# Optimization experiments

Hardware: AMD Instinct MI355X
Metric: run time of the kernel (lower is better)

## Reference

```python
import jax, jax.numpy as jnp
import numpy as np

N = 50000      # nodes
E = 800000     # edges
F_IN = 128     # numInputFeatures
HID = 64       # numHiddenLayerFeatures
C = 40         # numClasses


def setup_inputs() -> dict:
    key = jax.random.key(0)
    ks = jax.random.split(key, 24)
    def nrm(k, shape, s=0.05):
        return jax.random.normal(k, shape, jnp.float32) * s
    return {
        "x": jax.random.normal(ks[0], (N, F_IN), jnp.float32),
        "edge_index": jax.random.randint(ks[1], (2, E), 0, N, jnp.int64),
        "w": jax.random.normal(ks[2], (3,), jnp.float32),  # ensemble weights
        # GCNConv
        "W_gcn": nrm(ks[3], (F_IN, HID)), "b_gcn": jnp.zeros((HID,), jnp.float32),
        # SAGEConv (lin_l on aggregated neighbors w/ bias, lin_r on root no bias)
        "Wl_sage": nrm(ks[4], (F_IN, HID)), "bl_sage": jnp.zeros((HID,), jnp.float32),
        "Wr_sage": nrm(ks[5], (F_IN, HID)),
        # GATConv heads=1
        "W_gat": nrm(ks[6], (F_IN, HID)), "att_src": nrm(ks[7], (HID,)),
        "att_dst": nrm(ks[8], (HID,)), "b_gat": jnp.zeros((HID,), jnp.float32),
        # TransformerConv heads=1 (hidden -> classes)
        "Wq": nrm(ks[9], (HID, C)), "bq": jnp.zeros((C,), jnp.float32),
        "Wk": nrm(ks[10], (HID, C)), "bk": jnp.zeros((C,), jnp.float32),
        "Wv": nrm(ks[11], (HID, C)), "bv": jnp.zeros((C,), jnp.float32),
        "Wskip": nrm(ks[12], (HID, C)), "bskip": jnp.zeros((C,), jnp.float32),
    }


def _segment_softmax(e, seg, num_segments):
    m = jax.ops.segment_max(e, seg, num_segments=num_segments)
    ex = jnp.exp(e - m[seg])
    s = jax.ops.segment_sum(ex, seg, num_segments=num_segments)
    return ex / (s[seg] + 1e-16)


def _gcn(x, src, dst, W, b):
    h = x @ W                                        # [N, HID]
    loop = jnp.arange(N, dtype=src.dtype)
    s = jnp.concatenate([src, loop]); d = jnp.concatenate([dst, loop])
    deg = jax.ops.segment_sum(jnp.ones_like(d, jnp.float32), d, num_segments=N)
    dinv = jnp.where(deg > 0, jax.lax.rsqrt(deg), 0.0)
    norm = dinv[s] * dinv[d]                         # [E+N]
    out = jax.ops.segment_sum(h[s] * norm[:, None], d, num_segments=N)
    return out + b


def _sage(x, src, dst, Wl, bl, Wr):
    cnt = jax.ops.segment_sum(jnp.ones((src.shape[0],), jnp.float32), dst, num_segments=N)
    agg = jax.ops.segment_sum(x[src], dst, num_segments=N) / jnp.maximum(cnt, 1.0)[:, None]
    return agg @ Wl + bl + x @ Wr


def _gat(x, src, dst, W, att_src, att_dst, b):
    h = x @ W                                        # [N, HID]
    loop = jnp.arange(N, dtype=src.dtype)
    s = jnp.concatenate([src, loop]); d = jnp.concatenate([dst, loop])
    a_s = h @ att_src; a_d = h @ att_dst             # [N]
    e = jax.nn.leaky_relu(a_s[s] + a_d[d], 0.2)
    alpha = _segment_softmax(e, d, N)
    out = jax.ops.segment_sum(alpha[:, None] * h[s], d, num_segments=N)
    return out + b


def _transformer(x, src, dst, Wq, bq, Wk, bk, Wv, bv, Wskip, bskip):
    q = x @ Wq + bq; k = x @ Wk + bk; v = x @ Wv + bv  # [N, C]
    score = jnp.sum(q[dst] * k[src], axis=-1) / jnp.sqrt(jnp.float32(C))
    alpha = _segment_softmax(score, dst, N)
    out = jax.ops.segment_sum(alpha[:, None] * v[src], dst, num_segments=N)
    return out + (x @ Wskip + bskip)


def reference(x, edge_index, w, W_gcn, b_gcn, Wl_sage, bl_sage, Wr_sage,
              W_gat, att_src, att_dst, b_gat,
              Wq, bq, Wk, bk, Wv, bv, Wskip, bskip):
    src, dst = edge_index[0], edge_index[1]
    gelu = lambda t: jax.nn.gelu(t, approximate=False)
    ens = gelu(_gcn(x, src, dst, W_gcn, b_gcn)) * w[0]
    ens = ens + gelu(_sage(x, src, dst, Wl_sage, bl_sage, Wr_sage)) * w[1]
    ens = ens + gelu(_gat(x, src, dst, W_gat, att_src, att_dst, b_gat)) * w[2]
    out = _transformer(ens, src, dst, Wq, bq, Wk, bk, Wv, bv, Wskip, bskip)
    return jax.nn.log_softmax(out, axis=1)
```

## Files before the change

kernel.cpp:

```cpp
#include <hip/hip_runtime.h>
#include <math.h>

#define NN 50000
#define EE 800000
#define FIN 128
#define HID 64
#define CL 40
#define SCB 256
#define NBLK ((NN + SCB - 1) / SCB)
#define NREP 8
#define QW 256

typedef unsigned short ushort_t;
typedef unsigned int uint_t;
typedef float f32x2 __attribute__((ext_vector_type(2)));
typedef float f32x4 __attribute__((ext_vector_type(4)));
typedef short s16x8 __attribute__((ext_vector_type(8)));

#if defined(__has_builtin)
#if __has_builtin(__builtin_amdgcn_cvt_pk_f32_fp8)
#define HAVE_CVT_FP8 1
#endif
#endif

__device__ __forceinline__ ushort_t f2bf(float f) {
  uint_t u = __float_as_uint(f);
  u = (u + 0x7FFFu + ((u >> 16) & 1u)) >> 16;
  return (ushort_t)u;
}
__device__ __forceinline__ uint_t f2bf2(float lo, float hi) {
  return (uint_t)f2bf(lo) | ((uint_t)f2bf(hi) << 16);
}
__device__ __forceinline__ float bflo(uint_t u) {
  return __uint_as_float(u << 16);
}
__device__ __forceinline__ float bfhi(uint_t u) {
  return __uint_as_float(u & 0xFFFF0000u);
}

__device__ __forceinline__ uint_t f32_to_fp8(float f) {
  uint_t u = __float_as_uint(f);
  uint_t s = (u >> 31) << 7;
  uint_t mag = u & 0x7FFFFFFFu;
  if (mag < 0x3C800000u) return s;
  if (mag > 0x43E00000u) mag = 0x43E00000u;
  uint_t r = mag + 0x7FFFFu + ((mag >> 20) & 1u);
  if (r > 0x43E00000u) r = 0x43E00000u;
  return s | (((r - (120u << 23)) >> 20) & 0x7Fu);
}
__device__ __forceinline__ void fp8x4_to_f32(uint_t u, float* o) {
#ifdef HAVE_CVT_FP8
  f32x2 lo = __builtin_amdgcn_cvt_pk_f32_fp8(u, false);
  f32x2 hi = __builtin_amdgcn_cvt_pk_f32_fp8(u, true);
  o[0] = lo[0]; o[1] = lo[1]; o[2] = hi[0]; o[3] = hi[1];
#else
#pragma unroll
  for (int i = 0; i < 4; ++i) {
    uint_t b = (u >> (8 * i)) & 0xFFu;
    uint_t em = b & 0x7Fu;
    uint_t bits = ((b & 0x80u) << 24) | ((em << 20) + (120u << 23));
    o[i] = em ? __uint_as_float(bits) : 0.f;
  }
#endif
}

__device__ __forceinline__ int wave_sum_i(int v) {
#pragma unroll
  for (int off = 32; off > 0; off >>= 1) v += __shfl_xor(v, off, 64);
  return v;
}
__device__ __forceinline__ float wave_sum_f(float v) {
#pragma unroll
  for (int off = 32; off > 0; off >>= 1) v += __shfl_xor(v, off, 64);
  return v;
}
__device__ __forceinline__ float half_sum(float v) {
#pragma unroll
  for (int off = 16; off > 0; off >>= 1) v += __shfl_xor(v, off, 64);
  return v;
}
__device__ __forceinline__ float half_max(float v) {
#pragma unroll
  for (int off = 16; off > 0; off >>= 1) v = fmaxf(v, __shfl_xor(v, off, 64));
  return v;
}
__device__ __forceinline__ float gelu_exact(float x) {
  return 0.5f * x * (1.0f + erff(x * 0.70710678118654752f));
}
__device__ __forceinline__ float leaky02(float x) {
  return x >= 0.f ? x : 0.2f * x;
}

#define PREP_W 169
#define PREP_HIST 3125
#define PREP_X 12500
__global__ __launch_bounds__(256) void k_prep(
    const float* __restrict__ x, const int* __restrict__ dst,
    const float* __restrict__ W0, const float* __restrict__ W1,
    const float* __restrict__ W2, const float* __restrict__ W3,
    const float* __restrict__ Q0, const float* __restrict__ Q1,
    const float* __restrict__ Q2, const float* __restrict__ Q3,
    const float* __restrict__ b0, const float* __restrict__ b1,
    const float* __restrict__ b2, const float* __restrict__ b3,
    const float* __restrict__ attS, const float* __restrict__ attD,
    ushort_t* __restrict__ WtA, ushort_t* __restrict__ WtB,
    float* __restrict__ bcat, float* __restrict__ wv,
    int* __restrict__ cntR, int* __restrict__ erank,
    uint_t* __restrict__ xbu, ushort_t* __restrict__ xb8,
    float* __restrict__ a_s, float* __restrict__ a_d) {
  int b = blockIdx.x, t = threadIdx.x;
  if (b < PREP_W) {
    int idx = b * 256 + t;
    if (idx < 32768) {
      int m = idx >> 13, r = idx & 8191, c = r >> 7, k = r & 127;
      const float* W = (m == 0) ? W0 : (m == 1) ? W1 : (m == 2) ? W2 : W3;
      WtA[idx] = f2bf(W[k * HID + c]);
    } else if (idx < 43008) {
      int j = idx - 32768;
      int c = j >> 6, k = j & 63;
      int mm = c / CL, cc = c % CL;
      const float* W = (mm == 0) ? Q0 : (mm == 1) ? Q1 : (mm == 2) ? Q2 : Q3;
      WtB[j] = f2bf(W[k * CL + cc]);
    } else if (idx < 43168) {
      int c = idx - 43008;
      int mm = c / CL, cc = c % CL;
      const float* bb = (mm == 0) ? b0 : (mm == 1) ? b1 : (mm == 2) ? b2 : b3;
      bcat[c] = bb[cc];
    }
  } else if (b < PREP_W + PREP_HIST) {
    int hb = b - PREP_W;
    int e = hb * 256 + t;
    if (e < EE) {
      int r = hb & (NREP - 1);
      erank[e] = atomicAdd(&cntR[(size_t)r * NN + dst[e]], 1);
    }
  } else if (b < PREP_W + PREP_HIST + 1) {
    int which = t >> 7, k = t & 127;
    const float* att = which ? attD : attS;
    float s = 0.f;
    for (int c = 0; c < HID; ++c) s = fmaf(W2[k * HID + c], att[c], s);
    wv[which * FIN + k] = s;
  } else {
    int node = (b - PREP_W - PREP_HIST - 1) * 4 + (t >> 6);
    int l = t & 63;
    if (node < NN) {
      float2 xv = ((const float2*)x)[(size_t)node * 64 + l];
      float2 wsv = ((const float2*)wv)[l];
      float2 wdv = ((const float2*)(wv + FIN))[l];
      float ps = fmaf(xv.x, wsv.x, xv.y * wsv.y);
      float pd = fmaf(xv.x, wdv.x, xv.y * wdv.y);
      ps = wave_sum_f(ps);
      pd = wave_sum_f(pd);
      xbu[(size_t)node * 64 + l] = f2bf2(xv.x, xv.y);
      xb8[(size_t)node * 64 + l] =
          (ushort_t)(f32_to_fp8(xv.x) | (f32_to_fp8(xv.y) << 8));
      if (l == 0) { a_s[node] = ps; a_d[node] = pd; }
    }
  }
}

__global__ __launch_bounds__(SCB) void k_bsum(const int* __restrict__ cntR,
                                              int* __restrict__ bsum) {
  __shared__ int wsm[4];
  int i = blockIdx.x * SCB + threadIdx.x;
  int v = 0;
  if (i < NN) {
#pragma unroll
    for (int r = 0; r < NREP; ++r) v += cntR[(size_t)r * NN + i];
  }
  int s = wave_sum_i(v);
  int lane = threadIdx.x & 63, wv = threadIdx.x >> 6;
  if (lane == 0) wsm[wv] = s;
  __syncthreads();
  if (threadIdx.x == 0) bsum[blockIdx.x] = wsm[0] + wsm[1] + wsm[2] + wsm[3];
}

__global__ __launch_bounds__(SCB) void k_scanapply(
    const int* __restrict__ cntR, const int* __restrict__ bsum,
    const float* __restrict__ a_s, const float* __restrict__ a_d,
    int* __restrict__ cnt, int* __restrict__ offs, int* __restrict__ base8,
    float* __restrict__ dinv, float2* __restrict__ auxS,
    float2* __restrict__ auxD) {
  __shared__ int ts[SCB];
  __shared__ int wred[4];
  int b = blockIdx.x, t = threadIdx.x;
  int pv = (t < b) ? bsum[t] : 0;
  int ps = wave_sum_i(pv);
  int lane = t & 63, wv = t >> 6;
  if (lane == 0) wred[wv] = ps;
  int i = b * SCB + t;
  int cr[NREP];
  int v = 0;
  if (i < NN) {
#pragma unroll
    for (int r = 0; r < NREP; ++r) {
      cr[r] = cntR[(size_t)r * NN + i];
      v += cr[r];
    }
  }
  ts[t] = v;
  __syncthreads();
  int prefix = wred[0] + wred[1] + wred[2] + wred[3];
  for (int off = 1; off < SCB; off <<= 1) {
    int u = (t >= off) ? ts[t - off] : 0;
    __syncthreads();
    ts[t] += u;
    __syncthreads();
  }
  if (i < NN) {
    int ex = ts[t] - v + prefix;
    offs[i] = ex;
    cnt[i] = v;
    float dv = rsqrtf((float)v + 1.0f);
    dinv[i] = dv;
    auxS[i] = make_float2(dv, a_s[i]);
    auxD[i] = make_float2(dv, a_d[i]);
    int run = ex;
#pragma unroll
    for (int r = 0; r < NREP; ++r) {
      base8[(size_t)i * NREP + r] = run;
      run += cr[r];
    }
  }
}

__global__ __launch_bounds__(256) void k_sc1(const int* __restrict__ dst,
                                             const int* __restrict__ erank,
                                             const int* __restrict__ base8,
                                             int* __restrict__ esorted) {
  int e = blockIdx.x * blockDim.x + threadIdx.x;
  if (e < EE) {
    int d = dst[e];
    int r = (e >> 8) & (NREP - 1);
    esorted[base8[(size_t)d * NREP + r] + erank[e]] = e;
  }
}

__global__ __launch_bounds__(256) void k_sc2(
    const int* __restrict__ esorted, const int* __restrict__ src,
    const int* __restrict__ dst, const float2* __restrict__ auxS,
    const float2* __restrict__ auxD, int* __restrict__ srcidx,
    int* __restrict__ dsts, float2* __restrict__ edata) {
  int p = blockIdx.x * blockDim.x + threadIdx.x;
  if (p < EE) {
    int e = esorted[p];
    int s = src[e], d = dst[e];
    srcidx[p] = s;
    dsts[p] = d;
    float2 A = auxS[s];
    float2 B = auxD[d];
    float ex = __expf(leaky02(A.y + B.y));
    edata[p] = make_float2(A.x * B.x, ex);
  }
}

__global__ __launch_bounds__(256) void k_agg1x(
    const int* __restrict__ srcidx, const int* __restrict__ offs,
    const int* __restrict__ cnt, const uint_t* __restrict__ xb8u,
    const uint_t* __restrict__ xbu, const float2* __restrict__ edata,
    const float* __restrict__ dinv, const float* __restrict__ a_s,
    const float* __restrict__ a_d, uint_t* __restrict__ aggu) {
  int node = (blockIdx.x * blockDim.x + threadIdx.x) >> 6;
  int lane = threadIdx.x & 63;
  if (node >= NN) return;
  const int half = lane >> 5;
  const int fl = lane & 31;
  int beg = offs[node];
  int c = cnt[node];
  int end = beg + c;
  float g[4] = {0.f, 0.f, 0.f, 0.f};
  float sS[4] = {0.f, 0.f, 0.f, 0.f};
  float tA[4] = {0.f, 0.f, 0.f, 0.f};
  float dg = 0.f;
  int p = beg + half;
  for (; p + 6 < end; p += 8) {
    int s0 = srcidx[p], s1 = srcidx[p + 2], s2 = srcidx[p + 4],
        s3 = srcidx[p + 6];
    float2 e0 = edata[p], e1 = edata[p + 2], e2 = edata[p + 4],
           e3 = edata[p + 6];
    uint_t u0 = xb8u[(size_t)s0 * 32 + fl];
    uint_t u1 = xb8u[(size_t)s1 * 32 + fl];
    uint_t u2 = xb8u[(size_t)s2 * 32 + fl];
    uint_t u3 = xb8u[(size_t)s3 * 32 + fl];
    float A[4], B[4], C[4], D[4];
    fp8x4_to_f32(u0, A);
    fp8x4_to_f32(u1, B);
    fp8x4_to_f32(u2, C);
    fp8x4_to_f32(u3, D);
#pragma unroll
    for (int i = 0; i < 4; ++i) {
      g[i] = fmaf(A[i], e0.x, g[i]);
      g[i] = fmaf(B[i], e1.x, g[i]);
      g[i] = fmaf(C[i], e2.x, g[i]);
      g[i] = fmaf(D[i], e3.x, g[i]);
      sS[i] += (A[i] + B[i]) + (C[i] + D[i]);
      tA[i] = fmaf(A[i], e0.y, tA[i]);
      tA[i] = fmaf(B[i], e1.y, tA[i]);
      tA[i] = fmaf(C[i], e2.y, tA[i]);
      tA[i] = fmaf(D[i], e3.y, tA[i]);
    }
    dg += (e0.y + e1.y) + (e2.y + e3.y);
  }
  for (; p < end; p += 2) {
    int s0 = srcidx[p];
    float2 e0 = edata[p];
    uint_t u0 = xb8u[(size_t)s0 * 32 + fl];
    float A[4];
    fp8x4_to_f32(u0, A);
#pragma unroll
    for (int i = 0; i < 4; ++i) {
      g[i] = fmaf(A[i], e0.x, g[i]);
      sS[i] += A[i];
      tA[i] = fmaf(A[i], e0.y, tA[i]);
    }
    dg += e0.y;
  }
#pragma unroll
  for (int i = 0; i < 4; ++i) {
    g[i] += __shfl_xor(g[i], 32, 64);
    sS[i] += __shfl_xor(sS[i], 32, 64);
    tA[i] += __shfl_xor(tA[i], 32, 64);
  }
  dg += __shfl_xor(dg, 32, 64);
  float dd = dinv[node];
  float exl = __expf(leaky02(a_s[node] + a_d[node]));
  uint_t n0 = xbu[(size_t)node * 64 + 2 * fl];
  uint_t n1 = xbu[(size_t)node * 64 + 2 * fl + 1];
  float X[4] = {bflo(n0), bfhi(n0), bflo(n1), bfhi(n1)};
  float dd2 = dd * dd;
  float cinv = 1.0f / fmaxf((float)c, 1.0f);
  float gdi = 1.0f / (dg + exl + 1e-16f);
#pragma unroll
  for (int i = 0; i < 4; ++i) {
    g[i] = fmaf(X[i], dd2, g[i]);
    tA[i] = fmaf(X[i], exl, tA[i]);
    sS[i] *= cinv;
    tA[i] *= gdi;
  }
  if (half == 0) {
    uint_t* ag = aggu + (size_t)node * 192;
    ag[2 * fl] = f2bf2(g[0], g[1]);
    ag[2 * fl + 1] = f2bf2(g[2], g[3]);
    ag[64 + 2 * fl] = f2bf2(sS[0], sS[1]);
    ag[64 + 2 * fl + 1] = f2bf2(sS[2], sS[3]);
    ag[128 + 2 * fl] = f2bf2(tA[0], tA[1]);
    ag[128 + 2 * fl + 1] = f2bf2(tA[2], tA[3]);
  }
}

__global__ __launch_bounds__(256) void k_post(
    const ushort_t* __restrict__ agg, const ushort_t* __restrict__ xb,
    const ushort_t* __restrict__ WtA, const float* __restrict__ b_gcn,
    const float* __restrict__ bl, const float* __restrict__ b_gat,
    const float* __restrict__ w, ushort_t* __restrict__ ensb) {
  __shared__ __align__(16) ushort_t wlds[64 * 136];
  const int t = threadIdx.x;
  const int wv = t >> 6, l = t & 63;
  const int lr = l & 15, lg = l >> 4;
  const int rbase = blockIdx.x * 64 + wv * 16;
  int arow = rbase + lr;
  int arowc = arow < NN ? arow : NN - 1;
  f32x4 acc[4][4] = {};
#pragma unroll
  for (int m = 0; m < 4; ++m) {
    if (m) __syncthreads();
    for (int idx = t; idx < 64 * 16; idx += 256) {
      int c = idx >> 4, ch = idx & 15;
      *(uint4*)&wlds[c * 136 + ch * 8] =
          *(const uint4*)(WtA + m * 8192 + c * 128 + ch * 8);
    }
    __syncthreads();
    const ushort_t* ap = (m < 3) ? agg + (size_t)arowc * 384 + m * 128 + lg * 8
                                 : xb + (size_t)arowc * 128 + lg * 8;
#pragma unroll
    for (int ks = 0; ks < 4; ++ks) {
      s16x8 af = *(const s16x8*)(ap + ks * 32);
#pragma unroll
      for (int n = 0; n < 4; ++n) {
        s16x8 bf = *(const s16x8*)&wlds[(n * 16 + lr) * 136 + ks * 32 + lg * 8];
        acc[m][n] =
            __builtin_amdgcn_mfma_f32_16x16x32_bf16(af, bf, acc[m][n], 0, 0, 0);
      }
    }
  }
  float w0 = w[0], w1 = w[1], w2 = w[2];
#pragma unroll
  for (int n = 0; n < 4; ++n) {
    int col = n * 16 + lr;
    float bgv = b_gcn[col], bsv = bl[col], bav = b_gat[col];
#pragma unroll
    for (int j = 0; j < 4; ++j) {
      int orow = rbase + lg * 4 + j;
      if (orow < NN) {
        float g = gelu_exact(acc[0][n][j] + bgv);
        float s = gelu_exact(acc[1][n][j] + acc[3][n][j] + bsv);
        float tt = gelu_exact(acc[2][n][j] + bav);
        ensb[(size_t)orow * 64 + col] = f2bf(w0 * g + w1 * s + w2 * tt);
      }
    }
  }
}

__global__ __launch_bounds__(256) void k_gemmB(
    const ushort_t* __restrict__ ensb, const ushort_t* __restrict__ WtB,
    const float* __restrict__ bcat, ushort_t* __restrict__ QKVSb) {
  __shared__ __align__(16) ushort_t wb[160 * 72];
  __shared__ float bsh[160];
  const int t = threadIdx.x;
  for (int idx = t; idx < 160 * 8; idx += 256) {
    int c = idx >> 3, ch = idx & 7;
    *(uint4*)&wb[c * 72 + ch * 8] = *(const uint4*)(WtB + c * 64 + ch * 8);
  }
  if (t < 160) bsh[t] = bcat[t];
  __syncthreads();
  const int wv = t >> 6, l = t & 63;
  const int lr = l & 15, lg = l >> 4;
  const int rbase = blockIdx.x * 64 + wv * 16;
  int arow = rbase + lr;
  int arowc = arow < NN ? arow : NN - 1;
  const ushort_t* ap = ensb + (size_t)arowc * 64 + lg * 8;
  f32x4 acc[10] = {};
#pragma unroll
  for (int ks = 0; ks < 2; ++ks) {
    s16x8 af = *(const s16x8*)(ap + ks * 32);
#pragma unroll
    for (int n = 0; n < 10; ++n) {
      s16x8 bf = *(const s16x8*)&wb[(n * 16 + lr) * 72 + ks * 32 + lg * 8];
      acc[n] = __builtin_amdgcn_mfma_f32_16x16x32_bf16(af, bf, acc[n], 0, 0, 0);
    }
  }
#pragma unroll
  for (int n = 0; n < 10; ++n) {
    int col = n * 16 + lr;
    int seg = col / CL;
    int off = seg * 64 + (col - seg * CL);
#pragma unroll
    for (int j = 0; j < 4; ++j) {
      int orow = rbase + lg * 4 + j;
      if (orow < NN)
        QKVSb[(size_t)orow * QW + off] = f2bf(acc[n][j] + bsh[col]);
    }
  }
}

__global__ __launch_bounds__(256) void k_score(
    const int* __restrict__ srcidx, const int* __restrict__ dsts,
    const ushort_t* __restrict__ QKVSb, float* __restrict__ escore) {
  int p = blockIdx.x * 256 + threadIdx.x;
  if (p >= EE) return;
  int s = srcidx[p], d = dsts[p];
  const uint4* qp = (const uint4*)(QKVSb + (size_t)d * QW);
  const uint4* kp = (const uint4*)(QKVSb + (size_t)s * QW + 64);
  float dot = 0.f;
#pragma unroll
  for (int i = 0; i < 5; ++i) {
    uint4 q = qp[i], k = kp[i];
    dot = fmaf(bflo(q.x), bflo(k.x), dot);
    dot = fmaf(bfhi(q.x), bfhi(k.x), dot);
    dot = fmaf(bflo(q.y), bflo(k.y), dot);
    dot = fmaf(bfhi(q.y), bfhi(k.y), dot);
    dot = fmaf(bflo(q.z), bflo(k.z), dot);
    dot = fmaf(bfhi(q.z), bfhi(k.z), dot);
    dot = fmaf(bflo(q.w), bflo(k.w), dot);
    dot = fmaf(bfhi(q.w), bfhi(k.w), dot);
  }
  escore[p] = __expf(dot * 0.15811388300841897f);
}

__global__ __launch_bounds__(256) void k_agg2(
    const int* __restrict__ srcidx, const int* __restrict__ offs,
    const int* __restrict__ cnt, const ushort_t* __restrict__ QKVSb,
    const float* __restrict__ escore, float* __restrict__ out) {
  int node = (blockIdx.x * blockDim.x + threadIdx.x) >> 6;
  int lane = threadIdx.x & 63;
  if (node >= NN) return;
  const int half = lane >> 5;
  const int fl = lane & 31;
  const bool valid = fl < 20;
  int beg = offs[node];
  int end = beg + cnt[node];
  float den = 0.f, av0 = 0.f, av1 = 0.f;
  const int VOFF = 64;
  int p = beg + half;
  for (; p + 6 < end; p += 8) {
    int sA = srcidx[p], sB = srcidx[p + 2], sC = srcidx[p + 4],
        sD = srcidx[p + 6];
    float eA = escore[p], eB = escore[p + 2], eC = escore[p + 4],
          eD = escore[p + 6];
    uint_t vA = valid ? ((const uint_t*)QKVSb)[(size_t)sA * 128 + VOFF + fl] : 0u;
    uint_t vB = valid ? ((const uint_t*)QKVSb)[(size_t)sB * 128 + VOFF + fl] : 0u;
    uint_t vC = valid ? ((const uint_t*)QKVSb)[(size_t)sC * 128 + VOFF + fl] : 0u;
    uint_t vD = valid ? ((const uint_t*)QKVSb)[(size_t)sD * 128 + VOFF + fl] : 0u;
    av0 = fmaf(eA, bflo(vA), av0); av1 = fmaf(eA, bfhi(vA), av1);
    av0 = fmaf(eB, bflo(vB), av0); av1 = fmaf(eB, bfhi(vB), av1);
    av0 = fmaf(eC, bflo(vC), av0); av1 = fmaf(eC, bfhi(vC), av1);
    av0 = fmaf(eD, bflo(vD), av0); av1 = fmaf(eD, bfhi(vD), av1);
    den += (eA + eB) + (eC + eD);
  }
  for (; p < end; p += 2) {
    int sA = srcidx[p];
    float eA = escore[p];
    uint_t vA = valid ? ((const uint_t*)QKVSb)[(size_t)sA * 128 + VOFF + fl] : 0u;
    av0 = fmaf(eA, bflo(vA), av0); av1 = fmaf(eA, bfhi(vA), av1);
    den += eA;
  }
  av0 += __shfl_xor(av0, 32, 64);
  av1 += __shfl_xor(av1, 32, 64);
  den += __shfl_xor(den, 32, 64);
  uint_t sk = valid ? ((const uint_t*)QKVSb)[(size_t)node * 128 + 96 + fl] : 0u;
  float di = 1.0f / (den + 1e-16f);
  float o0 = valid ? av0 * di + bflo(sk) : -3.0e38f;
  float o1 = valid ? av1 * di + bfhi(sk) : -3.0e38f;
  float m = half_max(fmaxf(o0, o1));
  float eo = valid ? __expf(o0 - m) + __expf(o1 - m) : 0.f;
  float ls = logf(half_sum(eo));
  if (valid && half == 0) {
    float2 r = make_float2(o0 - m - ls, o1 - m - ls);
    ((float2*)out)[(size_t)node * 20 + fl] = r;
  }
}

extern "C" void kernel_launch(void* const* d_in, const int* in_sizes, int n_in,
                              void* d_out, int out_size, void* d_ws,
                              size_t ws_size, hipStream_t stream) {
  const float* x     = (const float*)d_in[0];
  const int*   ei    = (const int*)d_in[1];
  const float* w     = (const float*)d_in[2];
  const float* W_gcn = (const float*)d_in[3];
  const float* b_gcn = (const float*)d_in[4];
  const float* Wl    = (const float*)d_in[5];
  const float* bl    = (const float*)d_in[6];
  const float* Wr    = (const float*)d_in[7];
  const float* W_gat = (const float*)d_in[8];
  const float* att_s = (const float*)d_in[9];
  const float* att_d = (const float*)d_in[10];
  const float* b_gat = (const float*)d_in[11];
  const float* Wq    = (const float*)d_in[12];
  const float* bq    = (const float*)d_in[13];
  const float* Wk    = (const float*)d_in[14];
  const float* bk    = (const float*)d_in[15];
  const float* Wv    = (const float*)d_in[16];
  const float* bv    = (const float*)d_in[17];
  const float* Wsk   = (const float*)d_in[18];
  const float* bsk   = (const float*)d_in[19];
  float* out = (float*)d_out;
  float* ws  = (float*)d_ws;

  const int* src = ei;
  const int* dst = ei + EE;

  uint_t*   xbu    = (uint_t*)ws;
  uint_t*   aggu   = (uint_t*)(ws + (size_t)64 * NN);
  ushort_t* qkvsb  = (ushort_t*)(ws + (size_t)64 * NN);
  ushort_t* ensb   = (ushort_t*)(ws + (size_t)256 * NN);
  float*    a_s    = ws + (size_t)288 * NN;
  float*    a_d    = ws + (size_t)289 * NN;
  float*    dinv   = ws + (size_t)290 * NN;
  float2*   auxS   = (float2*)(ws + (size_t)291 * NN);
  float2*   auxD   = (float2*)(ws + (size_t)293 * NN);
  ushort_t* xb8    = (ushort_t*)(ws + (size_t)295 * NN);
  float*    wv     = ws + (size_t)327 * NN;
  ushort_t* WtA    = (ushort_t*)(ws + (size_t)327 * NN + 256);
  ushort_t* WtB    = (ushort_t*)(ws + (size_t)327 * NN + 16640);
  float*    bcat   = ws + (size_t)327 * NN + 21760;
  float*    escore = ws + (size_t)327 * NN + 21920;
  float2*   edata  = (float2*)(ws + (size_t)327 * NN + 21920 + EE);
  int*      ibase  = (int*)(ws + (size_t)327 * NN + 21920 + 3 * (size_t)EE);
  int*      cnt    = ibase;
  int*      offs   = ibase + NN;
  int*      srcidx = ibase + 2 * NN;
  int*      dsts   = ibase + 2 * NN + EE;
  int*      erank  = ibase + 2 * NN + 2 * EE;
  int*      esorted= ibase + 2 * NN + 3 * EE;
  int*      bsum   = ibase + 2 * NN + 4 * EE;
  int*      cntR   = ibase + 2 * NN + 4 * EE + 256;
  int*      base8  = cntR + (size_t)NREP * NN;

  hipMemsetAsync(cntR, 0, (size_t)NREP * NN * sizeof(int), stream);

  k_prep<<<PREP_W + PREP_HIST + 1 + PREP_X, 256, 0, stream>>>(
      x, dst, W_gcn, Wl, W_gat, Wr, Wq, Wk, Wv, Wsk, bq, bk, bv, bsk, att_s,
      att_d, WtA, WtB, bcat, wv, cntR, erank, xbu, xb8, a_s, a_d);

  k_bsum<<<NBLK, SCB, 0, stream>>>(cntR, bsum);
  k_scanapply<<<NBLK, SCB, 0, stream>>>(cntR, bsum, a_s, a_d, cnt, offs, base8,
                                        dinv, auxS, auxD);
  k_sc1<<<(EE + 255) / 256, 256, 0, stream>>>(dst, erank, base8, esorted);
  k_sc2<<<(EE + 255) / 256, 256, 0, stream>>>(esorted, src, dst, auxS, auxD,
                                              srcidx, dsts, edata);
  k_agg1x<<<(NN + 3) / 4, 256, 0, stream>>>(srcidx, offs, cnt, (uint_t*)xb8,
                                            xbu, edata, dinv, a_s, a_d, aggu);
  k_post<<<(NN + 63) / 64, 256, 0, stream>>>((const ushort_t*)aggu,
                                             (const ushort_t*)xbu, WtA, b_gcn,
                                             bl, b_gat, w, ensb);
  k_gemmB<<<(NN + 63) / 64, 256, 0, stream>>>(ensb, WtB, bcat, qkvsb);
  k_score<<<(EE + 255) / 256, 256, 0, stream>>>(srcidx, dsts, qkvsb, escore);
  k_agg2<<<(NN + 3) / 4, 256, 0, stream>>>(srcidx, offs, cnt, qkvsb, escore,
                                           out);
}
```

Before: 206.0 us.

## Replace global-atomic degree histogram with per-block LDS histograms for CSR build

Replaces the global atomic counting of edges per destination (8 replicated counters plus a memset) with a separate kernel where 64 blocks each build a 16-bit packed shared-memory histogram over two node-range passes. Each block writes its histogram to global memory, and the scan and scatter kernels then use per-block base offsets laid out block-major. This removes contended global atomics and the memset. In exchange, only 64 blocks run the histogram, and the scan now reads 64 entries per node instead of 8, which adds global traffic and serial work in the scan kernels.

```diff
diff --git a/kernel.cpp b/kernel.cpp
--- a/kernel.cpp
+++ b/kernel.cpp
@@ -8,7 +8,9 @@
 #define CL 40
 #define SCB 256
 #define NBLK ((NN + SCB - 1) / SCB)
-#define NREP 8
+#define NHB 64
+#define EPB 12500
+#define HRANGE 25000
 #define QW 256
 
 typedef unsigned short ushort_t;
@@ -92,10 +94,9 @@
 }
 
 #define PREP_W 169
-#define PREP_HIST 3125
 #define PREP_X 12500
 __global__ __launch_bounds__(256) void k_prep(
-    const float* __restrict__ x, const int* __restrict__ dst,
+    const float* __restrict__ x,
     const float* __restrict__ W0, const float* __restrict__ W1,
     const float* __restrict__ W2, const float* __restrict__ W3,
     const float* __restrict__ Q0, const float* __restrict__ Q1,
@@ -105,7 +106,6 @@
     const float* __restrict__ attS, const float* __restrict__ attD,
     ushort_t* __restrict__ WtA, ushort_t* __restrict__ WtB,
     float* __restrict__ bcat, float* __restrict__ wv,
-    int* __restrict__ cntR, int* __restrict__ erank,
     uint_t* __restrict__ xbu, ushort_t* __restrict__ xb8,
     float* __restrict__ a_s, float* __restrict__ a_d) {
   int b = blockIdx.x, t = threadIdx.x;
@@ -127,21 +127,14 @@
       const float* bb = (mm == 0) ? b0 : (mm == 1) ? b1 : (mm == 2) ? b2 : b3;
       bcat[c] = bb[cc];
     }
-  } else if (b < PREP_W + PREP_HIST) {
-    int hb = b - PREP_W;
-    int e = hb * 256 + t;
-    if (e < EE) {
-      int r = hb & (NREP - 1);
-      erank[e] = atomicAdd(&cntR[(size_t)r * NN + dst[e]], 1);
-    }
-  } else if (b < PREP_W + PREP_HIST + 1) {
+  } else if (b < PREP_W + 1) {
     int which = t >> 7, k = t & 127;
     const float* att = which ? attD : attS;
     float s = 0.f;
     for (int c = 0; c < HID; ++c) s = fmaf(W2[k * HID + c], att[c], s);
     wv[which * FIN + k] = s;
   } else {
-    int node = (b - PREP_W - PREP_HIST - 1) * 4 + (t >> 6);
+    int node = (b - PREP_W - 1) * 4 + (t >> 6);
     int l = t & 63;
     if (node < NN) {
       float2 xv = ((const float2*)x)[(size_t)node * 64 + l];
@@ -159,14 +152,40 @@
   }
 }
 
-__global__ __launch_bounds__(SCB) void k_bsum(const int* __restrict__ cntR,
+__global__ __launch_bounds__(256) void k_hist(const int* __restrict__ dst,
+                                              int* __restrict__ erank,
+                                              ushort_t* __restrict__ histG) {
+  __shared__ uint_t hl[HRANGE / 2];
+  int b = blockIdx.x, t = threadIdx.x;
+  int ebase = b * EPB;
+#pragma unroll 1
+  for (int pass = 0; pass < 2; ++pass) {
+    int lo = pass * HRANGE;
+    for (int i = t; i < HRANGE / 2; i += 256) hl[i] = 0;
+    __syncthreads();
+    for (int i = t; i < EPB; i += 256) {
+      int e = ebase + i;
+      int d = dst[e] - lo;
+      if (0 <= d && d < HRANGE) {
+        uint_t add = (d & 1) ? 0x10000u : 1u;
+        uint_t old = atomicAdd(&hl[d >> 1], add);
+        erank[e] = (d & 1) ? (int)(old >> 16) : (int)(old & 0xFFFFu);
+      }
+    }
+    __syncthreads();
+    uint_t* hg = (uint_t*)(histG + (size_t)b * NN + lo);
+    for (int i = t; i < HRANGE / 2; i += 256) hg[i] = hl[i];
+    __syncthreads();
+  }
+}
+
+__global__ __launch_bounds__(SCB) void k_bsum(const ushort_t* __restrict__ histG,
                                               int* __restrict__ bsum) {
   __shared__ int wsm[4];
   int i = blockIdx.x * SCB + threadIdx.x;
   int v = 0;
   if (i < NN) {
-#pragma unroll
-    for (int r = 0; r < NREP; ++r) v += cntR[(size_t)r * NN + i];
+    for (int r = 0; r < NHB; ++r) v += histG[(size_t)r * NN + i];
   }
   int s = wave_sum_i(v);
   int lane = threadIdx.x & 63, wv = threadIdx.x >> 6;
@@ -176,9 +195,9 @@
 }
 
 __global__ __launch_bounds__(SCB) void k_scanapply(
-    const int* __restrict__ cntR, const int* __restrict__ bsum,
+    const ushort_t* __restrict__ histG, const int* __restrict__ bsum,
     const float* __restrict__ a_s, const float* __restrict__ a_d,
-    int* __restrict__ cnt, int* __restrict__ offs, int* __restrict__ base8,
+    int* __restrict__ cnt, int* __restrict__ offs, int* __restrict__ baseT,
     float* __restrict__ dinv, float2* __restrict__ auxS,
     float2* __restrict__ auxD) {
   __shared__ int ts[SCB];
@@ -189,14 +208,9 @@
   int lane = t & 63, wv = t >> 6;
   if (lane == 0) wred[wv] = ps;
   int i = b * SCB + t;
-  int cr[NREP];
   int v = 0;
   if (i < NN) {
-#pragma unroll
-    for (int r = 0; r < NREP; ++r) {
-      cr[r] = cntR[(size_t)r * NN + i];
-      v += cr[r];
-    }
+    for (int r = 0; r < NHB; ++r) v += histG[(size_t)r * NN + i];
   }
   ts[t] = v;
   __syncthreads();
@@ -216,23 +230,22 @@
     auxS[i] = make_float2(dv, a_s[i]);
     auxD[i] = make_float2(dv, a_d[i]);
     int run = ex;
-#pragma unroll
-    for (int r = 0; r < NREP; ++r) {
-      base8[(size_t)i * NREP + r] = run;
-      run += cr[r];
+    for (int r = 0; r < NHB; ++r) {
+      baseT[(size_t)r * NN + i] = run;
+      run += histG[(size_t)r * NN + i];
     }
   }
 }
 
 __global__ __launch_bounds__(256) void k_sc1(const int* __restrict__ dst,
                                              const int* __restrict__ erank,
-                                             const int* __restrict__ base8,
+                                             const int* __restrict__ baseT,
                                              int* __restrict__ esorted) {
   int e = blockIdx.x * blockDim.x + threadIdx.x;
   if (e < EE) {
     int d = dst[e];
-    int r = (e >> 8) & (NREP - 1);
-    esorted[base8[(size_t)d * NREP + r] + erank[e]] = e;
+    int blk = e / EPB;
+    esorted[baseT[(size_t)blk * NN + d] + erank[e]] = e;
   }
 }
 
@@ -573,19 +586,17 @@
   int*      erank  = ibase + 2 * NN + 2 * EE;
   int*      esorted= ibase + 2 * NN + 3 * EE;
   int*      bsum   = ibase + 2 * NN + 4 * EE;
-  int*      cntR   = ibase + 2 * NN + 4 * EE + 256;
-  int*      base8  = cntR + (size_t)NREP * NN;
-
-  hipMemsetAsync(cntR, 0, (size_t)NREP * NN * sizeof(int), stream);
-
-  k_prep<<<PREP_W + PREP_HIST + 1 + PREP_X, 256, 0, stream>>>(
-      x, dst, W_gcn, Wl, W_gat, Wr, Wq, Wk, Wv, Wsk, bq, bk, bv, bsk, att_s,
-      att_d, WtA, WtB, bcat, wv, cntR, erank, xbu, xb8, a_s, a_d);
-
-  k_bsum<<<NBLK, SCB, 0, stream>>>(cntR, bsum);
-  k_scanapply<<<NBLK, SCB, 0, stream>>>(cntR, bsum, a_s, a_d, cnt, offs, base8,
-                                        dinv, auxS, auxD);
-  k_sc1<<<(EE + 255) / 256, 256, 0, stream>>>(dst, erank, base8, esorted);
+  ushort_t* histG  = (ushort_t*)(ibase + 2 * NN + 4 * EE + 256);
+  int*      baseT  = (int*)(histG + (size_t)NHB * NN);
+
+  k_prep<<<PREP_W + 1 + PREP_X, 256, 0, stream>>>(
+      x, W_gcn, Wl, W_gat, Wr, Wq, Wk, Wv, Wsk, bq, bk, bv, bsk, att_s, att_d,
+      WtA, WtB, bcat, wv, xbu, xb8, a_s, a_d);
+  k_hist<<<NHB, 256, 0, stream>>>(dst, erank, histG);
+  k_bsum<<<NBLK, SCB, 0, stream>>>(histG, bsum);
+  k_scanapply<<<NBLK, SCB, 0, stream>>>(histG, bsum, a_s, a_d, cnt, offs,
+                                        baseT, dinv, auxS, auxD);
+  k_sc1<<<(EE + 255) / 256, 256, 0, stream>>>(dst, erank, baseT, esorted);
   k_sc2<<<(EE + 255) / 256, 256, 0, stream>>>(esorted, src, dst, auxS, auxD,
                                               srcidx, dsts, edata);
   k_agg1x<<<(NN + 3) / 4, 256, 0, stream>>>(srcidx, offs, cnt, (uint_t*)xb8,
```

Measured after the change: 212.2 us. +3.0%, slower.
